# Kernel optimization log

Hardware: AMD Instinct MI355X
Metric: run time of the kernel (lower is better)

## Reference

```python
import jax, jax.numpy as jnp
import numpy as np

N_NODES = 100000
N_EDGES = 800000
DIM = 300
N_GRAPHS = 64
ATOM_VOCAB = 41
WORD_VOCAB = 10000


def setup_inputs() -> dict:
    key = jax.random.key(0)
    ks = jax.random.split(key, 7)
    atoms = jax.random.randint(ks[0], (N_NODES,), 0, ATOM_VOCAB)
    words = jax.random.randint(ks[1], (N_NODES,), 0, WORD_VOCAB)
    x = jnp.stack([atoms, words], axis=-1)  # [N,2] int indices
    edge_index = jax.random.randint(ks[2], (2, N_EDGES), 0, N_NODES)
    batch = jnp.sort(jax.random.randint(ks[3], (N_NODES,), 0, N_GRAPHS))
    atom_table = jax.random.normal(ks[4], (ATOM_VOCAB, DIM), dtype=jnp.float32) * 0.02
    word_table = jax.random.normal(ks[5], (WORD_VOCAB, DIM), dtype=jnp.float32) * 0.02
    W = jax.random.normal(ks[6], (DIM, DIM), dtype=jnp.float32) / np.sqrt(DIM)
    b = jnp.zeros((DIM,), dtype=jnp.float32)
    return {"x": x, "edge_index": edge_index, "batch": batch,
            "atom_table": atom_table, "word_table": word_table,
            "W": W, "b": b, "num_hops": 3}


def reference(x, edge_index, batch, atom_table, word_table, W, b, num_hops):
    n = x.shape[0]
    # GCNConv: add self-loops, symmetric degree normalization
    loops = jnp.arange(n)
    src = jnp.concatenate([edge_index[0], loops])  # [E+N]
    dst = jnp.concatenate([edge_index[1], loops])
    deg = jax.ops.segment_sum(jnp.ones_like(dst, dtype=W.dtype), dst, num_segments=n)
    dinv = jnp.where(deg > 0, jax.lax.rsqrt(deg), 0.0)
    norm = dinv[src] * dinv[dst]  # [E+N]

    # embed_nodes: atom embedding + word embedding
    h = atom_table[x[:, 0]] + word_table[x[:, 1]]  # [N, D]

    # num_hops applications of the SAME GCNConv (shared W, b)
    for _ in range(num_hops):
        hw = h @ W  # [N, D]
        msg = hw[src] * norm[:, None]  # [E+N, D]
        h = jax.ops.segment_sum(msg, dst, num_segments=n) + b

    # global_mean_pool over batch assignment
    sums = jax.ops.segment_sum(h, batch, num_segments=N_GRAPHS)  # [G, D]
    cnt = jax.ops.segment_sum(jnp.ones((n,), h.dtype), batch, num_segments=N_GRAPHS)
    return sums / jnp.maximum(cnt, 1.0)[:, None]
```

## Files before the change

### kernel.cpp

```cpp
#include <hip/hip_runtime.h>
#include <hip/hip_fp16.h>

#define NG 64
#define NGRAPH_C 64

#define RSZ 12500
#define RSZP 6250
#define NC_MS 64
#define MSB 1024

#define VOC 10000
#define KPAD 10240
#define NKC 80
#define WGK 128

#define NATOM 41
#define NC_A 128
#define ASL 128

__device__ __forceinline__ unsigned f_as_u(float f) { union { float f; unsigned u; } c; c.f = f; return c.u; }
__device__ __forceinline__ float u_as_f(unsigned u) { union { unsigned u; float f; } c; c.u = u; return c.f; }

__device__ __forceinline__ int xcc_id() {
    unsigned x;
    asm volatile("s_getreg_b32 %0, hwreg(HW_REG_XCC_ID)" : "=s"(x));
    return (int)(x & 7u);
}

union H4 { uint2 u2; __half h[4]; };

__global__ __launch_bounds__(MSB) void k_mscount(const int* __restrict__ src, const int* __restrict__ dst,
                                                 unsigned* __restrict__ rep_in,
                                                 unsigned* __restrict__ rep_src,
                                                 int e, int n, int chunk, int npairs) {
    __shared__ unsigned hin[RSZP];
    __shared__ unsigned hsrc[RSZP];
    int c = blockIdx.x % NC_MS;
    int r = blockIdx.x / NC_MS;
    int base = r * RSZ;
    int t = threadIdx.x;
    for (int w = t; w < RSZP; w += MSB) { hin[w] = 0u; hsrc[w] = 0u; }
    __syncthreads();
    int e0 = c * chunk, e1 = min(e, e0 + chunk);
    for (int i = e0 + t; i < e1; i += MSB) {
        int s = src[i], d = dst[i];
        unsigned ud = (unsigned)(d - base);
        unsigned us = (unsigned)(s - base);
        if (ud < (unsigned)RSZ) atomicAdd(&hin[ud >> 1], 1u << ((ud & 1) * 16));
        if (us < (unsigned)RSZ) atomicAdd(&hsrc[us >> 1], 1u << ((us & 1) * 16));
    }
    __syncthreads();
    int lim = min(RSZ, n - base);
    if (lim <= 0) return;
    int plim = (lim + 1) >> 1;
    unsigned* gin  = rep_in  + (size_t)c * npairs + (base >> 1);
    unsigned* gsrc = rep_src + (size_t)c * npairs + (base >> 1);
    for (int w = t; w < plim; w += MSB) { gin[w] = hin[w]; gsrc[w] = hsrc[w]; }
}

__global__ __launch_bounds__(256) void k_msreduce(const unsigned* __restrict__ rep_in,
                                                  unsigned* __restrict__ rep_src,
                                                  float* __restrict__ dinv,
                                                  unsigned* __restrict__ counts_src,
                                                  int n, int npairs) {
    int i2 = blockIdx.x * 256 + threadIdx.x;
    if (i2 >= npairs) return;
    unsigned slo = 0, shi = 0, rlo = 0, rhi = 0;
#pragma unroll 4
    for (int c = 0; c < NC_MS; ++c) {
        unsigned vi = rep_in[(size_t)c * npairs + i2];
        slo += vi & 0xFFFFu; shi += vi >> 16;
        unsigned vs = rep_src[(size_t)c * npairs + i2];
        rep_src[(size_t)c * npairs + i2] = rlo | (rhi << 16);
        rlo += vs & 0xFFFFu; rhi += vs >> 16;
    }
    int i = i2 * 2;
    dinv[i] = rsqrtf((float)(slo + 1u));
    counts_src[i] = rlo;
    if (i + 1 < n) {
        dinv[i + 1] = rsqrtf((float)(shi + 1u));
        counts_src[i + 1] = rhi;
    }
}

__global__ __launch_bounds__(256) void k_blocksum(const unsigned* __restrict__ counts,
                                                  unsigned* __restrict__ partials, int n) {
    __shared__ unsigned s[256];
    int base = blockIdx.x * 1024;
    unsigned sum = 0;
    for (int j = threadIdx.x; j < 1024; j += 256) {
        int i = base + j;
        sum += (i < n) ? counts[i] : 0u;
    }
    s[threadIdx.x] = sum;
    __syncthreads();
    for (int off = 128; off > 0; off >>= 1) {
        if (threadIdx.x < (unsigned)off) s[threadIdx.x] += s[threadIdx.x + off];
        __syncthreads();
    }
    if (threadIdx.x == 0) partials[blockIdx.x] = s[0];
}

__global__ __launch_bounds__(128) void k_scanpartials(unsigned* __restrict__ partials, int nb) {
    __shared__ unsigned s[128];
    int t = threadIdx.x;
    s[t] = (t < nb) ? partials[t] : 0u;
    __syncthreads();
    if (t == 0) {
        unsigned run = 0;
        for (int i = 0; i < nb; ++i) { unsigned v = s[i]; s[i] = run; run += v; }
    }
    __syncthreads();
    if (t < nb) partials[t] = s[t];
}

__global__ __launch_bounds__(256) void k_scanblock(const unsigned* __restrict__ counts,
                                                   const unsigned* __restrict__ partials,
                                                   unsigned* __restrict__ row_start, int n) {
    __shared__ unsigned s[256];
    int base = blockIdx.x * 1024;
    int t = threadIdx.x;
    unsigned v[4];
    unsigned tsum = 0;
#pragma unroll
    for (int j = 0; j < 4; ++j) {
        int i = base + t * 4 + j;
        v[j] = (i < n) ? counts[i] : 0u;
        tsum += v[j];
    }
    s[t] = tsum;
    __syncthreads();
    for (int off = 1; off < 256; off <<= 1) {
        unsigned x = (t >= off) ? s[t - off] : 0u;
        __syncthreads();
        s[t] += x;
        __syncthreads();
    }
    unsigned excl = (t > 0 ? s[t - 1] : 0u) + partials[blockIdx.x];
#pragma unroll
    for (int j = 0; j < 4; ++j) {
        int i = base + t * 4 + j;
        if (i < n) {
            row_start[i] = excl;
            excl += v[j];
            if (i == n - 1) row_start[n] = excl;
        }
    }
}

__global__ __launch_bounds__(MSB) void k_msfill(const int* __restrict__ src, const int* __restrict__ dst,
                                                const int* __restrict__ batch,
                                                const unsigned* __restrict__ row_start,
                                                const unsigned* __restrict__ pref,
                                                const float* __restrict__ dinv,
                                                uint2* __restrict__ euv,
                                                int e, int n, int chunk, int npairs) {
    __shared__ unsigned cur[RSZP];
    int c = blockIdx.x % NC_MS;
    int r = blockIdx.x / NC_MS;
    int base = r * RSZ;
    int t = threadIdx.x;
    for (int w = t; w < RSZP; w += MSB) cur[w] = 0u;
    __syncthreads();
    int e0 = c * chunk, e1 = min(e, e0 + chunk);
    const unsigned* prefc = pref + (size_t)c * npairs;
    for (int i = e0 + t; i < e1; i += MSB) {
        int s = src[i];
        unsigned us = (unsigned)(s - base);
        if (us < (unsigned)RSZ) {
            int d = dst[i];
            unsigned sh = (us & 1) * 16;
            unsigned old = atomicAdd(&cur[us >> 1], 1u << sh);
            unsigned slot = (old >> sh) & 0xFFFFu;
            unsigned p16 = (prefc[(unsigned)s >> 1] >> ((s & 1) * 16)) & 0xFFFFu;
            unsigned pos = row_start[s] + p16 + slot;
            uint2 pv;
            pv.x = (unsigned)d | ((unsigned)batch[d] << 17);
            pv.y = f_as_u(dinv[s] * dinv[d]);
            euv[pos] = pv;
        }
    }
}

__global__ __launch_bounds__(256) void k_wcount(const int* __restrict__ x,
                                                unsigned* __restrict__ wcnt, int n) {
    int j = blockIdx.x * 256 + threadIdx.x;
    if (j >= n) return;
    atomicAdd(&wcnt[x[2 * j + 1]], 1u);
}

__global__ __launch_bounds__(256) void k_wfill(const int* __restrict__ x,
                                               const unsigned* __restrict__ wstart,
                                               unsigned* __restrict__ wcur,
                                               unsigned* __restrict__ sorted, int n) {
    int j = blockIdx.x * 256 + threadIdx.x;
    if (j >= n) return;
    int w = x[2 * j + 1];
    unsigned pos = wstart[w] + atomicAdd(&wcur[w], 1u);
    sorted[pos] = (unsigned)j;
}

__global__ __launch_bounds__(256) void k_twfill(const __half* __restrict__ Y3,
                                                const unsigned* __restrict__ sorted,
                                                const unsigned* __restrict__ wstart,
                                                float* __restrict__ tw) {
    int w = blockIdx.x * 4 + (threadIdx.x >> 6);
    int g = threadIdx.x & 63;
    if (w >= VOC) return;
    unsigned i0 = wstart[w], i1 = wstart[w + 1];
    float s = 0.f;
    unsigned i = i0;
    for (; i + 2 <= i1; i += 2) {
        unsigned j0 = sorted[i], j1 = sorted[i + 1];
        s += __half2float(Y3[(size_t)j0 * NG + g]) + __half2float(Y3[(size_t)j1 * NG + g]);
    }
    if (i < i1) {
        unsigned j0 = sorted[i];
        s += __half2float(Y3[(size_t)j0 * NG + g]);
    }
    tw[(size_t)w * NG + g] = s;
}

__global__ __launch_bounds__(256) void k_amscount(const int* __restrict__ x,
                                                  unsigned* __restrict__ rep_a,
                                                  int n, int chunk) {
    __shared__ unsigned h[NATOM];
    int c = blockIdx.x;
    int t = threadIdx.x;
    if (t < NATOM) h[t] = 0u;
    __syncthreads();
    int j0 = c * chunk, j1 = min(n, j0 + chunk);
    for (int j = j0 + t; j < j1; j += 256) atomicAdd(&h[x[2 * j]], 1u);
    __syncthreads();
    if (t < NATOM) rep_a[c * NATOM + t] = h[t];
}

__global__ __launch_bounds__(64) void k_amsscan(unsigned* __restrict__ rep_a,
                                                unsigned* __restrict__ astart, int n) {
    __shared__ unsigned tot[NATOM];
    int t = threadIdx.x;
    if (t < NATOM) {
        unsigned run = 0;
        for (int c = 0; c < NC_A; ++c) {
            unsigned v = rep_a[c * NATOM + t];
            rep_a[c * NATOM + t] = run;
            run += v;
        }
        tot[t] = run;
    }
    __syncthreads();
    if (t == 0) {
        unsigned run = 0;
        for (int a = 0; a < NATOM; ++a) { astart[a] = run; run += tot[a]; }
        astart[NATOM] = run;
    }
}

__global__ __launch_bounds__(256) void k_amsfill(const int* __restrict__ x,
                                                 const unsigned* __restrict__ astart,
                                                 const unsigned* __restrict__ rep_a,
                                                 unsigned* __restrict__ asorted,
                                                 int n, int chunk) {
    __shared__ unsigned cur[NATOM];
    __shared__ unsigned base[NATOM];
    int c = blockIdx.x;
    int t = threadIdx.x;
    if (t < NATOM) {
        cur[t] = 0u;
        base[t] = astart[t] + rep_a[c * NATOM + t];
    }
    __syncthreads();
    int j0 = c * chunk, j1 = min(n, j0 + chunk);
    for (int j = j0 + t; j < j1; j += 256) {
        int a = x[2 * j];
        unsigned slot = atomicAdd(&cur[a], 1u);
        asorted[base[a] + slot] = (unsigned)j;
    }
}

__global__ __launch_bounds__(256) void k_tafill(const __half* __restrict__ Y3,
                                                const unsigned* __restrict__ asorted,
                                                const unsigned* __restrict__ astart,
                                                float* __restrict__ tap) {
    int wid = blockIdx.x * 4 + (threadIdx.x >> 6);
    if (wid >= NATOM * ASL) return;
    int a  = wid >> 7;
    int sl = wid & (ASL - 1);
    int g  = threadIdx.x & 63;
    unsigned i0 = astart[a], i1 = astart[a + 1];
    unsigned len = i1 - i0;
    unsigned lo = i0 + (unsigned)((unsigned long long)len * sl / ASL);
    unsigned hi = i0 + (unsigned)((unsigned long long)len * (sl + 1) / ASL);
    float s = 0.f;
    unsigned i = lo;
    for (; i + 2 <= hi; i += 2) {
        unsigned j0 = asorted[i], j1 = asorted[i + 1];
        s += __half2float(Y3[(size_t)j0 * NG + g]) + __half2float(Y3[(size_t)j1 * NG + g]);
    }
    if (i < hi) s += __half2float(Y3[(size_t)asorted[i] * NG + g]);
    tap[((size_t)a * ASL + sl) * NG + g] = s;
}

__global__ __launch_bounds__(256) void k_tareduce(const float* __restrict__ tap,
                                                  float* __restrict__ ta) {
    int i = blockIdx.x * 256 + threadIdx.x;
    if (i >= NATOM * NG) return;
    int a = i >> 6;
    int g = i & 63;
    float s = 0.f;
    for (int sl = 0; sl < ASL; ++sl) s += tap[((size_t)a * ASL + sl) * NG + g];
    ta[i] = s;
}

__global__ __launch_bounds__(128) void k_gstart(const int* __restrict__ batch,
                                                int* __restrict__ gstart, int n, int ngraph) {
    int g = threadIdx.x;
    if (g > ngraph) return;
    if (g == ngraph) { gstart[g] = n; return; }
    int lo = 0, hi = n;
    while (lo < hi) {
        int mid = (lo + hi) >> 1;
        if (batch[mid] < g) lo = mid + 1; else hi = mid;
    }
    gstart[g] = lo;
}

__global__ __launch_bounds__(256) void k_y1(const int* __restrict__ batch,
                                            const float* __restrict__ dinv,
                                            const unsigned* __restrict__ row_start,
                                            const uint2* __restrict__ euv,
                                            __half* __restrict__ Y1, int n) {
    int idx = blockIdx.x * 256 + threadIdx.x;
    if (idx >= n * 16) return;
    int j = idx >> 4;
    int c4 = idx & 15;
    int cb = c4 * 4;
    float a0 = 0.f, a1 = 0.f, a2 = 0.f, a3 = 0.f;
    {
        int bj = batch[j];
        float dj = dinv[j];
        float sn = dj * dj;
        a0 += (bj == cb + 0) ? sn : 0.f;
        a1 += (bj == cb + 1) ? sn : 0.f;
        a2 += (bj == cb + 2) ? sn : 0.f;
        a3 += (bj == cb + 3) ? sn : 0.f;
    }
    unsigned e0 = row_start[j], e1 = row_start[j + 1];
    unsigned e = e0;
    for (; e + 4 <= e1; e += 4) {
        uint2 p0 = euv[e], p1 = euv[e + 1], p2 = euv[e + 2], p3 = euv[e + 3];
        int b0 = (int)(p0.x >> 17), b1 = (int)(p1.x >> 17);
        int b2 = (int)(p2.x >> 17), b3 = (int)(p3.x >> 17);
        float v0 = u_as_f(p0.y), v1 = u_as_f(p1.y);
        float v2 = u_as_f(p2.y), v3 = u_as_f(p3.y);
        a0 += ((b0 == cb + 0) ? v0 : 0.f) + ((b1 == cb + 0) ? v1 : 0.f)
            + ((b2 == cb + 0) ? v2 : 0.f) + ((b3 == cb + 0) ? v3 : 0.f);
        a1 += ((b0 == cb + 1) ? v0 : 0.f) + ((b1 == cb + 1) ? v1 : 0.f)
            + ((b2 == cb + 1) ? v2 : 0.f) + ((b3 == cb + 1) ? v3 : 0.f);
        a2 += ((b0 == cb + 2) ? v0 : 0.f) + ((b1 == cb + 2) ? v1 : 0.f)
            + ((b2 == cb + 2) ? v2 : 0.f) + ((b3 == cb + 2) ? v3 : 0.f);
        a3 += ((b0 == cb + 3) ? v0 : 0.f) + ((b1 == cb + 3) ? v1 : 0.f)
            + ((b2 == cb + 3) ? v2 : 0.f) + ((b3 == cb + 3) ? v3 : 0.f);
    }
    for (; e < e1; ++e) {
        uint2 p = euv[e];
        int bd = (int)(p.x >> 17);
        float v = u_as_f(p.y);
        a0 += (bd == cb + 0) ? v : 0.f;
        a1 += (bd == cb + 1) ? v : 0.f;
        a2 += (bd == cb + 2) ? v : 0.f;
        a3 += (bd == cb + 3) ? v : 0.f;
    }
    H4 o;
    o.h[0] = __float2half(a0); o.h[1] = __float2half(a1);
    o.h[2] = __float2half(a2); o.h[3] = __float2half(a3);
    *(uint2*)&Y1[(size_t)j * NG + cb] = o.u2;
}

__global__ __launch_bounds__(256) void k_yprop(const __half* __restrict__ Yin,
                                               const float* __restrict__ dinv,
                                               const unsigned* __restrict__ row_start,
                                               const uint2* __restrict__ euv,
                                               __half* __restrict__ Yout, int n) {
    int idx = blockIdx.x * 256 + threadIdx.x;
    if (idx >= n * 16) return;
    int j = idx >> 4;
    int c4 = idx & 15;
    int cb = c4 * 4;
    float dj = dinv[j];
    float sn = dj * dj;
    H4 s; s.u2 = *(const uint2*)&Yin[(size_t)j * NG + cb];
    float a0 = sn * __half2float(s.h[0]);
    float a1 = sn * __half2float(s.h[1]);
    float a2 = sn * __half2float(s.h[2]);
    float a3 = sn * __half2float(s.h[3]);
    unsigned e0 = row_start[j], e1 = row_start[j + 1];
    unsigned e = e0;
    for (; e + 4 <= e1; e += 4) {
        uint2 p0 = euv[e], p1 = euv[e + 1], p2 = euv[e + 2], p3 = euv[e + 3];
        float v0 = u_as_f(p0.y), v1 = u_as_f(p1.y);
        float v2 = u_as_f(p2.y), v3 = u_as_f(p3.y);
        H4 m0; m0.u2 = *(const uint2*)&Yin[(size_t)(p0.x & 0x1FFFFu) * NG + cb];
        H4 m1; m1.u2 = *(const uint2*)&Yin[(size_t)(p1.x & 0x1FFFFu) * NG + cb];
        H4 m2; m2.u2 = *(const uint2*)&Yin[(size_t)(p2.x & 0x1FFFFu) * NG + cb];
        H4 m3; m3.u2 = *(const uint2*)&Yin[(size_t)(p3.x & 0x1FFFFu) * NG + cb];
        a0 += v0 * __half2float(m0.h[0]) + v1 * __half2float(m1.h[0])
            + v2 * __half2float(m2.h[0]) + v3 * __half2float(m3.h[0]);
        a1 += v0 * __half2float(m0.h[1]) + v1 * __half2float(m1.h[1])
            + v2 * __half2float(m2.h[1]) + v3 * __half2float(m3.h[1]);
        a2 += v0 * __half2float(m0.h[2]) + v1 * __half2float(m1.h[2])
            + v2 * __half2float(m2.h[2]) + v3 * __half2float(m3.h[2]);
        a3 += v0 * __half2float(m0.h[3]) + v1 * __half2float(m1.h[3])
            + v2 * __half2float(m2.h[3]) + v3 * __half2float(m3.h[3]);
    }
    for (; e < e1; ++e) {
        uint2 p0 = euv[e];
        float v0 = u_as_f(p0.y);
        H4 m0; m0.u2 = *(const uint2*)&Yin[(size_t)(p0.x & 0x1FFFFu) * NG + cb];
        a0 += v0 * __half2float(m0.h[0]);
        a1 += v0 * __half2float(m0.h[1]);
        a2 += v0 * __half2float(m0.h[2]);
        a3 += v0 * __half2float(m0.h[3]);
    }
    H4 o;
    o.h[0] = __float2half(a0); o.h[1] = __float2half(a1);
    o.h[2] = __float2half(a2); o.h[3] = __float2half(a3);
    *(uint2*)&Yout[(size_t)j * NG + cb] = o.u2;
}

__global__ __launch_bounds__(256) void k_colsumh(const __half* __restrict__ Y,
                                                 float* __restrict__ su8, int n) {
    __shared__ float red[16][NG];
    int t = threadIdx.x;
    int cg = t & 15;
    int sr = t >> 4;
    float a0 = 0.f, a1 = 0.f, a2 = 0.f, a3 = 0.f;
    int stride = gridDim.x * 16;
    for (int j = blockIdx.x * 16 + sr; j < n; j += stride) {
        H4 v; v.u2 = *(const uint2*)&Y[(size_t)j * NG + cg * 4];
        a0 += __half2float(v.h[0]);
        a1 += __half2float(v.h[1]);
        a2 += __half2float(v.h[2]);
        a3 += __half2float(v.h[3]);
    }
    red[sr][cg * 4 + 0] = a0;
    red[sr][cg * 4 + 1] = a1;
    red[sr][cg * 4 + 2] = a2;
    red[sr][cg * 4 + 3] = a3;
    __syncthreads();
    if (t < NG) {
        float s = 0.f;
#pragma unroll
        for (int q = 0; q < 16; ++q) s += red[q][t];
        int r = xcc_id();
        __hip_atomic_fetch_add(&su8[r * NG + t], s,
                               __ATOMIC_RELAXED, __HIP_MEMORY_SCOPE_WORKGROUP);
    }
}

__global__ __launch_bounds__(256) void k_wgemm2(const float* __restrict__ T,
                                                const float* __restrict__ Tab,
                                                float* __restrict__ Gpart) {
    __shared__ float Asm[32 * 64];
    __shared__ float Bsm[32 * 64];
    const int t = threadIdx.x;
    const int tg = t >> 4;
    const int tc = t & 15;
    const int c0 = blockIdx.x * 64;
    const int kb = blockIdx.y * WGK;

    float acc[4][4] = {};

    for (int sub = 0; sub < WGK / 32; ++sub) {
        int kbase = kb + sub * 32;
#pragma unroll
        for (int r2 = 0; r2 < 2; ++r2) {
            int idx4 = r2 * 256 + t;
            int k = idx4 >> 4, g4 = idx4 & 15;
            float4 v = *(const float4*)&T[(size_t)(kbase + k) * 64 + g4 * 4];
            *(float4*)&Asm[k * 64 + g4 * 4] = v;
        }
#pragma unroll
        for (int r2 = 0; r2 < 2; ++r2) {
            int idx4 = r2 * 256 + t;
            int k = idx4 >> 4, c4i = idx4 & 15;
            int gk = kbase + k;
            int cb2 = c0 + c4i * 4;
            float4 v;
            if (gk < VOC && cb2 + 3 < 300) {
                v = *(const float4*)&Tab[(size_t)gk * 300 + cb2];
            } else {
                float tmp[4];
#pragma unroll
                for (int q = 0; q < 4; ++q)
                    tmp[q] = (gk < VOC && cb2 + q < 300) ? Tab[(size_t)gk * 300 + cb2 + q] : 0.f;
                v.x = tmp[0]; v.y = tmp[1]; v.z = tmp[2]; v.w = tmp[3];
            }
            *(float4*)&Bsm[k * 64 + c4i * 4] = v;
        }
        __syncthreads();
#pragma unroll 8
        for (int k = 0; k < 32; ++k) {
            float4 a4 = *(const float4*)&Asm[k * 64 + tg * 4];
            float4 b4 = *(const float4*)&Bsm[k * 64 + tc * 4];
            float a[4] = {a4.x, a4.y, a4.z, a4.w};
            float b[4] = {b4.x, b4.y, b4.z, b4.w};
#pragma unroll
            for (int i = 0; i < 4; ++i)
#pragma unroll
                for (int jj = 0; jj < 4; ++jj) acc[i][jj] += a[i] * b[jj];
        }
        __syncthreads();
    }

    float* gp = Gpart + (size_t)blockIdx.y * (NG * 300);
#pragma unroll
    for (int i = 0; i < 4; ++i) {
        int g = tg * 4 + i;
#pragma unroll
        for (int jj = 0; jj < 4; ++jj) {
            int c = c0 + tc * 4 + jj;
            if (c < 300) gp[g * 300 + c] = acc[i][jj];
        }
    }
}

__global__ __launch_bounds__(256) void k_greduce(const float* __restrict__ Gpart,
                                                 float* __restrict__ G0) {
    int k = blockIdx.x * 256 + threadIdx.x;
    if (k >= NG * 300) return;
    int p0 = blockIdx.y * (NKC / 8);
    int p1 = p0 + (NKC / 8);
    float s = 0.f;
    for (int p = p0; p < p1; ++p) s += Gpart[(size_t)p * (NG * 300) + k];
    atomicAdd(&G0[k], s);
}

__global__ __launch_bounds__(256) void k_agemm(const float* __restrict__ T,
                                               const float* __restrict__ Tab,
                                               float* __restrict__ G0) {
    int j = blockIdx.x * 256 + threadIdx.x;
    if (j >= NG * 300) return;
    int g = j / 300, c = j - g * 300;
    float acc = 0.f;
#pragma unroll
    for (int k = 0; k < 41; ++k) acc += T[(size_t)k * NG + g] * Tab[(size_t)k * 300 + c];
    atomicAdd(&G0[j], acc);
}

__global__ __launch_bounds__(256) void k_smm(const float* __restrict__ A,
                                             const float* __restrict__ W,
                                             float* __restrict__ C) {
    int j = blockIdx.x * 256 + threadIdx.x;
    if (j >= NG * 300) return;
    int g = j / 300, c = j - g * 300;
    int k0 = blockIdx.y * 60;
    float acc = 0.f;
#pragma unroll 1
    for (int k = k0; k < k0 + 60; k += 4) {
        float a0 = A[g * 300 + k + 0], a1 = A[g * 300 + k + 1];
        float a2 = A[g * 300 + k + 2], a3 = A[g * 300 + k + 3];
        float w0 = W[(k + 0) * 300 + c], w1 = W[(k + 1) * 300 + c];
        float w2 = W[(k + 2) * 300 + c], w3 = W[(k + 3) * 300 + c];
        acc += a0 * w0 + a1 * w1 + a2 * w2 + a3 * w3;
    }
    atomicAdd(&C[j], acc);
}

__global__ __launch_bounds__(256) void k_vec(const float* __restrict__ vin,
                                             const float* __restrict__ W,
                                             float* __restrict__ r_out) {
    int c = blockIdx.x * 256 + threadIdx.x;
    if (c >= 300) return;
    int k0 = blockIdx.y * 75;
    float acc = 0.f;
    for (int k = k0; k < k0 + 75; ++k) acc += vin[k] * W[k * 300 + c];
    atomicAdd(&r_out[c], acc);
}

__global__ __launch_bounds__(256) void k_out(const float* __restrict__ T3,
                                             const float* __restrict__ su1,
                                             const float* __restrict__ su2,
                                             const int* __restrict__ gstart,
                                             const float* __restrict__ r1,
                                             const float* __restrict__ r2,
                                             const float* __restrict__ b,
                                             float* __restrict__ out) {
    int j = blockIdx.x * 256 + threadIdx.x;
    if (j >= NG * 300) return;
    int g = j / 300, c = j - g * 300;
    int cnt = gstart[g + 1] - gstart[g];
    float s1 = 0.f, s2 = 0.f;
#pragma unroll
    for (int r = 0; r < 8; ++r) {
        s1 += su1[r * NG + g];
        s2 += su2[r * NG + g];
    }
    float v = T3[j] + s2 * r2[c] + s1 * r1[c] + (float)cnt * b[c];
    out[j] = v / (float)(cnt > 0 ? cnt : 1);
}

extern "C" void kernel_launch(void* const* d_in, const int* in_sizes, int n_in,
                              void* d_out, int out_size, void* d_ws, size_t ws_size,
                              hipStream_t stream) {
    const int*   x     = (const int*)d_in[0];
    const int*   ei    = (const int*)d_in[1];
    const int*   batch = (const int*)d_in[2];
    const float* at    = (const float*)d_in[3];
    const float* wt    = (const float*)d_in[4];
    const float* W     = (const float*)d_in[5];
    const float* b     = (const float*)d_in[6];

    const int n = in_sizes[0] / 2;
    const int e = in_sizes[1] / 2;

    char* ws = (char*)d_ws;
    size_t off = 0;
    auto carve = [&](size_t bytes) {
        void* p = ws + off;
        off += (bytes + 255) & ~(size_t)255;
        return p;
    };
    __half*   Y1        = (__half*)carve((size_t)n * NG * 2);
    __half*   Y2        = (__half*)carve((size_t)n * NG * 2);
    __half*   Y3        = (__half*)carve((size_t)n * NG * 2);
    uint2*    euv       = (uint2*)carve((size_t)e * 8);
    float*    dinv      = (float*)carve((size_t)n * 4);
    unsigned* counts_src= (unsigned*)carve((size_t)n * 4);
    unsigned* row_start = (unsigned*)carve((size_t)(n + 1) * 4);
    unsigned* partials  = (unsigned*)carve(1024 * 4);
    int*      gstart    = (int*)carve(65 * 4);
    unsigned* wstart    = (unsigned*)carve((size_t)(VOC + 1) * 4);
    unsigned* sorted    = (unsigned*)carve((size_t)n * 4);
    unsigned* asorted   = (unsigned*)carve((size_t)n * 4);
    unsigned* astart    = (unsigned*)carve((NATOM + 1) * 4);
    unsigned* rep_a     = (unsigned*)carve((size_t)NC_A * NATOM * 4);
    float*    tap       = (float*)carve((size_t)NATOM * ASL * NG * 4);
    char*     zB0       = (char*)carve(0);
    float*    su1       = (float*)carve((size_t)8 * NG * 4);
    float*    su2       = (float*)carve((size_t)8 * NG * 4);
    float*    ta        = (float*)carve((size_t)NATOM * NG * 4);
    float*    tw        = (float*)carve((size_t)KPAD * NG * 4);
    float*    G0        = (float*)carve((size_t)NG * 300 * 4);
    float*    r1        = (float*)carve(300 * 4);
    float*    r2        = (float*)carve(300 * 4);
    float*    T1        = (float*)carve((size_t)NG * 300 * 4);
    float*    T2        = (float*)carve((size_t)NG * 300 * 4);
    float*    T3        = (float*)carve((size_t)NG * 300 * 4);
    unsigned* wcnt      = (unsigned*)carve((size_t)VOC * 4);
    unsigned* wcur      = (unsigned*)carve((size_t)VOC * 4);
    char*     zB1       = (char*)carve(0);

    const int* src = ei;
    const int* dst = ei + e;

    unsigned* rep_in  = (unsigned*)Y1;
    unsigned* rep_src = (unsigned*)Y2;
    float*    Gpart   = (float*)Y1;

    hipMemsetAsync(zB0, 0, (size_t)(zB1 - zB0), stream);

    const int npairs = (n + 1) / 2;
    const int NRng   = (n + RSZ - 1) / RSZ;
    const int chunk  = (e + NC_MS - 1) / NC_MS;
    const int achunk = (n + NC_A - 1) / NC_A;

    k_mscount<<<NRng * NC_MS, MSB, 0, stream>>>(src, dst, rep_in, rep_src, e, n, chunk, npairs);
    k_msreduce<<<(npairs + 255) / 256, 256, 0, stream>>>(rep_in, rep_src, dinv, counts_src, n, npairs);
    int NB = (n + 1023) / 1024;
    k_blocksum<<<NB, 256, 0, stream>>>(counts_src, partials, n);
    k_scanpartials<<<1, 128, 0, stream>>>(partials, NB);
    k_scanblock<<<NB, 256, 0, stream>>>(counts_src, partials, row_start, n);
    k_msfill<<<NRng * NC_MS, MSB, 0, stream>>>(src, dst, batch, row_start, rep_src, dinv, euv, e, n, chunk, npairs);
    k_gstart<<<1, 128, 0, stream>>>(batch, gstart, n, NGRAPH_C);

    int nb256 = (n + 255) / 256;
    k_wcount<<<nb256, 256, 0, stream>>>(x, wcnt, n);
    int NBW = (VOC + 1023) / 1024;
    k_blocksum<<<NBW, 256, 0, stream>>>(wcnt, partials, VOC);
    k_scanpartials<<<1, 128, 0, stream>>>(partials, NBW);
    k_scanblock<<<NBW, 256, 0, stream>>>(wcnt, partials, wstart, VOC);
    k_wfill<<<nb256, 256, 0, stream>>>(x, wstart, wcur, sorted, n);

    k_amscount<<<NC_A, 256, 0, stream>>>(x, rep_a, n, achunk);
    k_amsscan<<<1, 64, 0, stream>>>(rep_a, astart, n);
    k_amsfill<<<NC_A, 256, 0, stream>>>(x, astart, rep_a, asorted, n, achunk);

    int yb = (n * 16 + 255) / 256;
    k_y1<<<yb, 256, 0, stream>>>(batch, dinv, row_start, euv, Y1, n);
    k_colsumh<<<512, 256, 0, stream>>>(Y1, su1, n);
    k_yprop<<<yb, 256, 0, stream>>>(Y1, dinv, row_start, euv, Y2, n);
    k_colsumh<<<512, 256, 0, stream>>>(Y2, su2, n);
    k_yprop<<<yb, 256, 0, stream>>>(Y2, dinv, row_start, euv, Y3, n);

    k_tafill<<<(NATOM * ASL + 3) / 4, 256, 0, stream>>>(Y3, asorted, astart, tap);
    k_tareduce<<<(NATOM * NG + 255) / 256, 256, 0, stream>>>(tap, ta);
    k_twfill<<<(VOC + 3) / 4, 256, 0, stream>>>(Y3, sorted, wstart, tw);
    {
        dim3 gw(5, NKC);
        k_wgemm2<<<gw, 256, 0, stream>>>(tw, wt, Gpart);
        dim3 gr((NG * 300 + 255) / 256, 8);
        k_greduce<<<gr, 256, 0, stream>>>(Gpart, G0);
    }
    k_agemm<<<(NG * 300 + 255) / 256, 256, 0, stream>>>(ta, at, G0);

    {
        dim3 gs((NG * 300 + 255) / 256, 5);
        k_smm<<<gs, 256, 0, stream>>>(G0, W, T1);
        k_smm<<<gs, 256, 0, stream>>>(T1, W, T2);
        k_smm<<<gs, 256, 0, stream>>>(T2, W, T3);
        dim3 gv(2, 4);
        k_vec<<<gv, 256, 0, stream>>>(b, W, r1);
        k_vec<<<gv, 256, 0, stream>>>(r1, W, r2);
    }

    k_out<<<(NG * 300 + 255) / 256, 256, 0, stream>>>(T3, su1, su2, gstart, r1, r2, b, (float*)d_out);
}
```

Measured before the change: 325.3 us.

## Pack edge histograms as 8-bit counters, widen ranges, single-kernel word scan

Result: no change. 325.1 us (-0.1%).

```diff
diff --git a/kernel.cpp b/kernel.cpp
--- a/kernel.cpp
+++ b/kernel.cpp
@@ -4,15 +4,16 @@
 #define NG 64
 #define NGRAPH_C 64
 
-#define RSZ 12500
-#define RSZP 6250
-#define NC_MS 64
+#define RSZ 25000
+#define RSZP4 6250
+#define NC_MS 128
+#define NRNG 4
 #define MSB 1024
 
 #define VOC 10000
 #define KPAD 10240
-#define NKC 80
-#define WGK 128
+#define NKC 160
+#define WGK 64
 
 #define NATOM 41
 #define NC_A 128
@@ -32,29 +33,29 @@
 __global__ __launch_bounds__(MSB) void k_mscount(const int* __restrict__ src, const int* __restrict__ dst,
                                                  unsigned* __restrict__ rep_in,
                                                  unsigned* __restrict__ rep_src,
-                                                 int e, int n, int chunk, int npairs) {
-    __shared__ unsigned hin[RSZP];
-    __shared__ unsigned hsrc[RSZP];
+                                                 int e, int n, int chunk, int nwords) {
+    __shared__ unsigned hin[RSZP4];
+    __shared__ unsigned hsrc[RSZP4];
     int c = blockIdx.x % NC_MS;
     int r = blockIdx.x / NC_MS;
     int base = r * RSZ;
     int t = threadIdx.x;
-    for (int w = t; w < RSZP; w += MSB) { hin[w] = 0u; hsrc[w] = 0u; }
+    for (int w = t; w < RSZP4; w += MSB) { hin[w] = 0u; hsrc[w] = 0u; }
     __syncthreads();
     int e0 = c * chunk, e1 = min(e, e0 + chunk);
     for (int i = e0 + t; i < e1; i += MSB) {
         int s = src[i], d = dst[i];
         unsigned ud = (unsigned)(d - base);
         unsigned us = (unsigned)(s - base);
-        if (ud < (unsigned)RSZ) atomicAdd(&hin[ud >> 1], 1u << ((ud & 1) * 16));
-        if (us < (unsigned)RSZ) atomicAdd(&hsrc[us >> 1], 1u << ((us & 1) * 16));
+        if (ud < (unsigned)RSZ) atomicAdd(&hin[ud >> 2], 1u << ((ud & 3) * 8));
+        if (us < (unsigned)RSZ) atomicAdd(&hsrc[us >> 2], 1u << ((us & 3) * 8));
     }
     __syncthreads();
     int lim = min(RSZ, n - base);
     if (lim <= 0) return;
-    int plim = (lim + 1) >> 1;
-    unsigned* gin  = rep_in  + (size_t)c * npairs + (base >> 1);
-    unsigned* gsrc = rep_src + (size_t)c * npairs + (base >> 1);
+    int plim = (lim + 3) >> 2;
+    unsigned* gin  = rep_in  + (size_t)c * nwords + (base >> 2);
+    unsigned* gsrc = rep_src + (size_t)c * nwords + (base >> 2);
     for (int w = t; w < plim; w += MSB) { gin[w] = hin[w]; gsrc[w] = hsrc[w]; }
 }
 
@@ -62,24 +63,28 @@
                                                   unsigned* __restrict__ rep_src,
                                                   float* __restrict__ dinv,
                                                   unsigned* __restrict__ counts_src,
-                                                  int n, int npairs) {
-    int i2 = blockIdx.x * 256 + threadIdx.x;
-    if (i2 >= npairs) return;
-    unsigned slo = 0, shi = 0, rlo = 0, rhi = 0;
+                                                  int n, int nwords) {
+    int i4 = blockIdx.x * 256 + threadIdx.x;
+    if (i4 >= nwords) return;
+    unsigned s0 = 0, s1 = 0, s2 = 0, s3 = 0;
+    unsigned r0 = 0, r1 = 0, r2 = 0, r3 = 0;
 #pragma unroll 4
     for (int c = 0; c < NC_MS; ++c) {
-        unsigned vi = rep_in[(size_t)c * npairs + i2];
-        slo += vi & 0xFFFFu; shi += vi >> 16;
-        unsigned vs = rep_src[(size_t)c * npairs + i2];
-        rep_src[(size_t)c * npairs + i2] = rlo | (rhi << 16);
-        rlo += vs & 0xFFFFu; rhi += vs >> 16;
-    }
-    int i = i2 * 2;
-    dinv[i] = rsqrtf((float)(slo + 1u));
-    counts_src[i] = rlo;
-    if (i + 1 < n) {
-        dinv[i + 1] = rsqrtf((float)(shi + 1u));
-        counts_src[i + 1] = rhi;
+        unsigned vi = rep_in[(size_t)c * nwords + i4];
+        s0 += vi & 0xFFu; s1 += (vi >> 8) & 0xFFu; s2 += (vi >> 16) & 0xFFu; s3 += vi >> 24;
+        unsigned vs = rep_src[(size_t)c * nwords + i4];
+        rep_src[(size_t)c * nwords + i4] = r0 | (r1 << 8) | (r2 << 16) | (r3 << 24);
+        r0 += vs & 0xFFu; r1 += (vs >> 8) & 0xFFu; r2 += (vs >> 16) & 0xFFu; r3 += vs >> 24;
+    }
+    int i = i4 * 4;
+    unsigned sv[4] = {s0, s1, s2, s3};
+    unsigned rv[4] = {r0, r1, r2, r3};
+#pragma unroll
+    for (int q = 0; q < 4; ++q) {
+        if (i + q < n) {
+            dinv[i + q] = rsqrtf((float)(sv[q] + 1u));
+            counts_src[i + q] = rv[q];
+        }
     }
 }
 
@@ -154,26 +159,26 @@
                                                 const unsigned* __restrict__ pref,
                                                 const float* __restrict__ dinv,
                                                 uint2* __restrict__ euv,
-                                                int e, int n, int chunk, int npairs) {
-    __shared__ unsigned cur[RSZP];
+                                                int e, int n, int chunk, int nwords) {
+    __shared__ unsigned cur[RSZP4];
     int c = blockIdx.x % NC_MS;
     int r = blockIdx.x / NC_MS;
     int base = r * RSZ;
     int t = threadIdx.x;
-    for (int w = t; w < RSZP; w += MSB) cur[w] = 0u;
+    for (int w = t; w < RSZP4; w += MSB) cur[w] = 0u;
     __syncthreads();
     int e0 = c * chunk, e1 = min(e, e0 + chunk);
-    const unsigned* prefc = pref + (size_t)c * npairs;
+    const unsigned* prefc = pref + (size_t)c * nwords;
     for (int i = e0 + t; i < e1; i += MSB) {
         int s = src[i];
         unsigned us = (unsigned)(s - base);
         if (us < (unsigned)RSZ) {
             int d = dst[i];
-            unsigned sh = (us & 1) * 16;
-            unsigned old = atomicAdd(&cur[us >> 1], 1u << sh);
-            unsigned slot = (old >> sh) & 0xFFFFu;
-            unsigned p16 = (prefc[(unsigned)s >> 1] >> ((s & 1) * 16)) & 0xFFFFu;
-            unsigned pos = row_start[s] + p16 + slot;
+            unsigned sh = (us & 3) * 8;
+            unsigned old = atomicAdd(&cur[us >> 2], 1u << sh);
+            unsigned slot = (old >> sh) & 0xFFu;
+            unsigned p8 = (prefc[(unsigned)s >> 2] >> ((s & 3) * 8)) & 0xFFu;
+            unsigned pos = row_start[s] + p8 + slot;
             uint2 pv;
             pv.x = (unsigned)d | ((unsigned)batch[d] << 17);
             pv.y = f_as_u(dinv[s] * dinv[d]);
@@ -187,6 +192,33 @@
     int j = blockIdx.x * 256 + threadIdx.x;
     if (j >= n) return;
     atomicAdd(&wcnt[x[2 * j + 1]], 1u);
+}
+
+__global__ __launch_bounds__(1024) void k_wscan(const unsigned* __restrict__ wcnt,
+                                                unsigned* __restrict__ wstart) {
+    __shared__ unsigned s[1024];
+    int t = threadIdx.x;
+    int lo = t * 10;
+    unsigned v[10];
+    unsigned sum = 0;
+    if (lo < VOC) {
+#pragma unroll
+        for (int q = 0; q < 10; ++q) { v[q] = wcnt[lo + q]; sum += v[q]; }
+    }
+    s[t] = sum;
+    __syncthreads();
+    for (int off = 1; off < 1024; off <<= 1) {
+        unsigned x = (t >= off) ? s[t - off] : 0u;
+        __syncthreads();
+        s[t] += x;
+        __syncthreads();
+    }
+    if (lo < VOC) {
+        unsigned excl = (t > 0) ? s[t - 1] : 0u;
+#pragma unroll
+        for (int q = 0; q < 10; ++q) { wstart[lo + q] = excl; excl += v[q]; }
+    }
+    if (t == 1023) wstart[VOC] = s[1023];
 }
 
 __global__ __launch_bounds__(256) void k_wfill(const int* __restrict__ x,
@@ -660,26 +692,22 @@
 
     hipMemsetAsync(zB0, 0, (size_t)(zB1 - zB0), stream);
 
-    const int npairs = (n + 1) / 2;
-    const int NRng   = (n + RSZ - 1) / RSZ;
+    const int nwords = (n + 3) / 4;
     const int chunk  = (e + NC_MS - 1) / NC_MS;
     const int achunk = (n + NC_A - 1) / NC_A;
 
-    k_mscount<<<NRng * NC_MS, MSB, 0, stream>>>(src, dst, rep_in, rep_src, e, n, chunk, npairs);
-    k_msreduce<<<(npairs + 255) / 256, 256, 0, stream>>>(rep_in, rep_src, dinv, counts_src, n, npairs);
+    k_mscount<<<NRNG * NC_MS, MSB, 0, stream>>>(src, dst, rep_in, rep_src, e, n, chunk, nwords);
+    k_msreduce<<<(nwords + 255) / 256, 256, 0, stream>>>(rep_in, rep_src, dinv, counts_src, n, nwords);
     int NB = (n + 1023) / 1024;
     k_blocksum<<<NB, 256, 0, stream>>>(counts_src, partials, n);
     k_scanpartials<<<1, 128, 0, stream>>>(partials, NB);
     k_scanblock<<<NB, 256, 0, stream>>>(counts_src, partials, row_start, n);
-    k_msfill<<<NRng * NC_MS, MSB, 0, stream>>>(src, dst, batch, row_start, rep_src, dinv, euv, e, n, chunk, npairs);
+    k_msfill<<<NRNG * NC_MS, MSB, 0, stream>>>(src, dst, batch, row_start, rep_src, dinv, euv, e, n, chunk, nwords);
     k_gstart<<<1, 128, 0, stream>>>(batch, gstart, n, NGRAPH_C);
 
     int nb256 = (n + 255) / 256;
     k_wcount<<<nb256, 256, 0, stream>>>(x, wcnt, n);
-    int NBW = (VOC + 1023) / 1024;
-    k_blocksum<<<NBW, 256, 0, stream>>>(wcnt, partials, VOC);
-    k_scanpartials<<<1, 128, 0, stream>>>(partials, NBW);
-    k_scanblock<<<NBW, 256, 0, stream>>>(wcnt, partials, wstart, VOC);
+    k_wscan<<<1, 1024, 0, stream>>>(wcnt, wstart);
     k_wfill<<<nb256, 256, 0, stream>>>(x, wstart, wcur, sorted, n);
 
     k_amscount<<<NC_A, 256, 0, stream>>>(x, rep_a, n, achunk);
```
